# Performance work log

Hardware: AMD Instinct MI355X
Metric: run time of the kernel (lower is better)

## Reference

```python
import jax, jax.numpy as jnp
import numpy as np

HIDDEN = 2048
NUM_HEADS = 16
HEAD_DIM = HIDDEN // NUM_HEADS  # 128
ROPE_THETA = 10000.0
T = 4096


def _rope(x, positions):
    # x: [T, H, D]; neox-style rotary (rotate halves), matching vLLM get_rope default
    half = HEAD_DIM // 2
    inv_freq = 1.0 / (ROPE_THETA ** (jnp.arange(0, half, dtype=jnp.float32) / half))
    freqs = positions.astype(jnp.float32)[:, None] * inv_freq[None, :]  # [T, half]
    cos = jnp.cos(freqs)[:, None, :]  # [T, 1, half]
    sin = jnp.sin(freqs)[:, None, :]
    x1, x2 = x[..., :half], x[..., half:]
    return jnp.concatenate([x1 * cos - x2 * sin, x2 * cos + x1 * sin], axis=-1)


def setup_inputs() -> dict:
    key = jax.random.key(0)
    k1, k2, k3 = jax.random.split(key, 3)
    return {
        "hidden_states": jax.random.normal(k1, (T, HIDDEN), dtype=jnp.float32),
        "positions": jnp.arange(T, dtype=jnp.int32),
        "w_qkv": jax.random.normal(k2, (HIDDEN, 3 * HIDDEN), dtype=jnp.float32) * (HIDDEN ** -0.5),
        "w_o": jax.random.normal(k3, (HIDDEN, HIDDEN), dtype=jnp.float32) * (HIDDEN ** -0.5),
    }


def reference(hidden_states, positions, w_qkv, w_o):
    qkv = hidden_states @ w_qkv  # [T, 3H]
    q, k, v = jnp.split(qkv, 3, axis=-1)
    q = q.reshape(T, NUM_HEADS, HEAD_DIM)
    k = k.reshape(T, NUM_HEADS, HEAD_DIM)
    v = v.reshape(T, NUM_HEADS, HEAD_DIM)
    q = _rope(q, positions)
    k = _rope(k, positions)
    scale = HEAD_DIM ** -0.5
    # causal SDPA over flattened single sequence
    scores = jnp.einsum("qhd,khd->hqk", q, k) * scale  # [H, T, T]
    causal = jnp.tril(jnp.ones((T, T), dtype=bool))
    scores = jnp.where(causal[None, :, :], scores, jnp.finfo(scores.dtype).min)
    probs = jax.nn.softmax(scores, axis=-1)
    attn = jnp.einsum("hqk,khd->qhd", probs, v).reshape(T, HIDDEN)
    return attn @ w_o
```

## Files before the change

kernel.cpp:

```cpp
#include <hip/hip_runtime.h>
#include <hip/hip_bf16.h>
#include <cstdint>
#include <cstddef>

#define T_SEQ 4096
#define HID   2048
#define NH    16
#define HD    128
#define QKVN  6144
#define KVB   32
#define CHT   16
#define CPH   144

typedef unsigned short u16;
typedef unsigned int u32;
typedef __bf16 bf16x8 __attribute__((ext_vector_type(8)));
typedef float  f32x4  __attribute__((ext_vector_type(4)));

typedef const __attribute__((address_space(1))) void* gas_ptr;
typedef __attribute__((address_space(3))) void* las_ptr;

__device__ __forceinline__ void async16(const void* g, void* l) {
  __builtin_amdgcn_global_load_lds((gas_ptr)g, (las_ptr)l, 16, 0, 0);
}

__device__ __forceinline__ u16 f2bf(float f) {
  unsigned int u = __float_as_uint(f);
  u += 0x7fffu + ((u >> 16) & 1u);
  return (u16)(u >> 16);
}

__device__ __forceinline__ float bf2f(u16 x) {
  return __uint_as_float((unsigned)x << 16);
}

__global__ void cast_f32_bf16(const float* __restrict__ in, u16* __restrict__ out, int n) {
  int i = (blockIdx.x * blockDim.x + threadIdx.x) * 4;
  if (i >= n) return;
  float4 v = *(const float4*)&in[i];
  uint2 o;
  o.x = (unsigned)f2bf(v.x) | ((unsigned)f2bf(v.y) << 16);
  o.y = (unsigned)f2bf(v.z) | ((unsigned)f2bf(v.w) << 16);
  *(uint2*)&out[i] = o;
}

__global__ void transpose_cast(const float* __restrict__ in, u16* __restrict__ out,
                               int R, int C) {
  __shared__ float tile[64][65];
  int c0 = blockIdx.x * 64, r0 = blockIdx.y * 64;
  int tid = threadIdx.x;
#pragma unroll
  for (int i = 0; i < 16; ++i) {
    int e = i * 256 + tid;
    int rr = e >> 6, cc = e & 63;
    tile[rr][cc] = in[(size_t)(r0 + rr) * C + c0 + cc];
  }
  __syncthreads();
#pragma unroll
  for (int i = 0; i < 16; ++i) {
    int e = i * 256 + tid;
    int oc = e >> 6, orr = e & 63;
    out[(size_t)(c0 + oc) * R + r0 + orr] = f2bf(tile[orr][oc]);
  }
}

template <typename OUT>
__global__ __launch_bounds__(256)
void gemm_bf16_bt(const u16* __restrict__ A, const u16* __restrict__ BT,
                  OUT* __restrict__ C, int M, int N, int K) {
  __shared__ u16 As[2][128 * 32];
  __shared__ u16 Bs[2][128 * 32];
  int tid = threadIdx.x;
  int row0 = blockIdx.y * 128, col0 = blockIdx.x * 128;
  int wv = tid >> 6, lane = tid & 63, lr = lane & 15, lq = lane >> 4;
  int wm = (wv >> 1) * 64, wn = (wv & 1) * 64;
  f32x4 acc[4][4] = {};

  auto stage = [&](int buf, int ks) {
#pragma unroll
    for (int k = 0; k < 2; ++k) {
      int c = k * 256 + tid;
      int row = c >> 2, col = c & 3;
      int key = (row >> 1) & 3;
      async16(&A[(size_t)(row0 + row) * K + ks + (col ^ key) * 8], &As[buf][c * 8]);
      async16(&BT[(size_t)(col0 + row) * K + ks + (col ^ key) * 8], &Bs[buf][c * 8]);
    }
  };

  stage(0, 0);
  __syncthreads();
  int nk = K >> 5;
  for (int t = 0; t < nk; ++t) {
    int cur = t & 1;
    if (t + 1 < nk) stage(cur ^ 1, (t + 1) * 32);

    const char* AsB = (const char*)&As[cur][0];
    const char* BsB = (const char*)&Bs[cur][0];
    bf16x8 a[4], b[4];
#pragma unroll
    for (int mi = 0; mi < 4; ++mi) {
      int row = wm + mi * 16 + lr;
      a[mi] = *(const bf16x8*)(AsB + row * 64 + ((lq ^ ((row >> 1) & 3)) << 4));
    }
#pragma unroll
    for (int ni = 0; ni < 4; ++ni) {
      int row = wn + ni * 16 + lr;
      b[ni] = *(const bf16x8*)(BsB + row * 64 + ((lq ^ ((row >> 1) & 3)) << 4));
    }
#pragma unroll
    for (int mi = 0; mi < 4; ++mi)
#pragma unroll
      for (int ni = 0; ni < 4; ++ni)
        acc[mi][ni] = __builtin_amdgcn_mfma_f32_16x16x32_bf16(a[mi], b[ni], acc[mi][ni], 0, 0, 0);
    __syncthreads();
  }

#pragma unroll
  for (int mi = 0; mi < 4; ++mi)
#pragma unroll
    for (int ni = 0; ni < 4; ++ni)
#pragma unroll
      for (int r = 0; r < 4; ++r) {
        float v = acc[mi][ni][r];
        size_t idx = (size_t)(row0 + wm + mi * 16 + lq * 4 + r) * N + col0 + wn + ni * 16 + lr;
        if constexpr (sizeof(OUT) == 2) C[idx] = (OUT)f2bf(v);
        else                            C[idx] = (OUT)v;
      }
}

#define SCL2 0.12753224f

__global__ void rope_reorg(const u16* __restrict__ qkv, const int* __restrict__ pos,
                           u16* __restrict__ Qh, u16* __restrict__ Kh) {
  int idx = blockIdx.x * 256 + threadIdx.x;
  if (idx >= T_SEQ * NH * 64) return;
  int d = idx & 63;
  int h = (idx >> 6) & (NH - 1);
  int t = idx >> 10;
  float p = (float)pos[t];
  float inv = exp2f((float)d * -0.20762050594046932f);
  float f = p * inv;
  float s, c;
  __sincosf(f, &s, &c);

  size_t ib = (size_t)t * QKVN + h * HD + d;
  float q1 = bf2f(qkv[ib]), q2 = bf2f(qkv[ib + 64]);
  float k1 = bf2f(qkv[ib + HID]), k2 = bf2f(qkv[ib + HID + 64]);
  size_t ob = ((size_t)h * T_SEQ + t) * HD + d;
  Qh[ob]      = f2bf((q1 * c - q2 * s) * SCL2);
  Qh[ob + 64] = f2bf((q2 * c + q1 * s) * SCL2);
  Kh[ob]      = f2bf(k1 * c - k2 * s);
  Kh[ob + 64] = f2bf(k2 * c + k1 * s);
}

__global__ void vtrans(const u16* __restrict__ qkv, u16* __restrict__ Vt) {
  __shared__ u16 tile[64][136];
  int t0 = blockIdx.x * 64;
  int h = blockIdx.y;
  int tid = threadIdx.x;
#pragma unroll
  for (int i = 0; i < 32; ++i) {
    int e = i * 256 + tid;
    int tt = e >> 7, d = e & 127;
    tile[tt][d] = qkv[(size_t)(t0 + tt) * QKVN + 2 * HID + h * HD + d];
  }
  __syncthreads();
#pragma unroll
  for (int i = 0; i < 32; ++i) {
    int e = i * 256 + tid;
    int d = e >> 6, tt = e & 63;
    Vt[((size_t)h * HD + d) * T_SEQ + t0 + tt] = tile[tt][d];
  }
}

__global__ __launch_bounds__(256)
void attn_fwd(const u16* __restrict__ Qh, const u16* __restrict__ Kh,
              const u16* __restrict__ Vt, u16* __restrict__ Opart,
              float2* __restrict__ ml) {
  __shared__ u16 Ks[2][32 * 128];
  __shared__ u16 Vs[2][128 * 32];
  __shared__ u16 Ps[4][32 * 32];

  int tid = threadIdx.x;
  int wv = tid >> 6, lane = tid & 63, lr = lane & 15, lq = lane >> 4;
  char* PsB = (char*)&Ps[wv][0];

  int id = blockIdx.x;
  int h = id / CPH;
  int w = id - h * CPH;
  int bq = 0, acc = 0;
  for (;;) {
    int ch = (bq + 4) >> 2;
    if (w < acc + ch) break;
    acc += ch;
    ++bq;
  }
  int c = w - acc;
  int nt = 4 * bq + 4;
  int j0 = c * CHT, j1 = min(j0 + CHT, nt);
  int q0 = bq * 128, wrow0 = q0 + wv * 32;

  bf16x8 qf[2][4];
#pragma unroll
  for (int mi = 0; mi < 2; ++mi)
#pragma unroll
    for (int kd = 0; kd < 4; ++kd)
      qf[mi][kd] = *(const bf16x8*)
          &Qh[((size_t)h * T_SEQ + wrow0 + mi * 16 + lr) * HD + kd * 32 + lq * 8];

  f32x4 acc_o[2][8] = {};
  float m_run[2][4], l_run[2][4];
#pragma unroll
  for (int mi = 0; mi < 2; ++mi)
#pragma unroll
    for (int r = 0; r < 4; ++r) { m_run[mi][r] = -1e30f; l_run[mi][r] = 0.0f; }

  auto stage = [&](int buf, int jb) {
#pragma unroll
    for (int k = 0; k < 2; ++k) {
      int cc = k * 256 + tid;
      int row = cc >> 4;
      int sc = (cc ^ (row & 7)) & 15;
      async16(&Kh[((size_t)h * T_SEQ + jb + row) * HD + sc * 8], &Ks[buf][cc * 8]);
    }
#pragma unroll
    for (int k = 0; k < 2; ++k) {
      int cc = k * 256 + tid;
      int row = cc >> 2, col = cc & 3;
      int key = (row >> 1) & 3;
      async16(&Vt[((size_t)h * HD + row) * T_SEQ + jb + (col ^ key) * 8],
              &Vs[buf][cc * 8]);
    }
  };

  stage(0, j0 * KVB);
  __syncthreads();

  for (int j = j0; j < j1; ++j) {
    int cur = (j - j0) & 1;
    int jb = j * KVB;
    if (j + 1 < j1) stage(cur ^ 1, jb + KVB);

    if (jb <= wrow0 + 31) {
      const char* KsB = (const char*)&Ks[cur][0];
      const char* VsB = (const char*)&Vs[cur][0];

      f32x4 s_acc[2][2] = {};
#pragma unroll
      for (int kd = 0; kd < 4; ++kd) {
#pragma unroll
        for (int nj = 0; nj < 2; ++nj) {
          int row = nj * 16 + lr;
          int byt = (row << 8) + kd * 64 + lq * 16;
          bf16x8 kf = *(const bf16x8*)(KsB + (byt ^ ((row & 7) << 4)));
#pragma unroll
          for (int mi = 0; mi < 2; ++mi)
            s_acc[mi][nj] = __builtin_amdgcn_mfma_f32_16x16x32_bf16(
                qf[mi][kd], kf, s_acc[mi][nj], 0, 0, 0);
        }
      }

      bool diag = (jb + KVB - 1 > wrow0);
#pragma unroll
      for (int mi = 0; mi < 2; ++mi) {
        float pm[4];
#pragma unroll
        for (int r = 0; r < 4; ++r) {
          int qrow = wrow0 + mi * 16 + lq * 4 + r;
          float mx = -1e30f;
#pragma unroll
          for (int nj = 0; nj < 2; ++nj) {
            float sv = s_acc[mi][nj][r];
            if (diag && (jb + nj * 16 + lr > qrow)) sv = -1e30f;
            s_acc[mi][nj][r] = sv;
            mx = fmaxf(mx, sv);
          }
          pm[r] = mx;
        }
#pragma unroll
        for (int r = 0; r < 4; ++r) {
          pm[r] = fmaxf(pm[r], __shfl_xor(pm[r], 1));
          pm[r] = fmaxf(pm[r], __shfl_xor(pm[r], 2));
          pm[r] = fmaxf(pm[r], __shfl_xor(pm[r], 4));
          pm[r] = fmaxf(pm[r], __shfl_xor(pm[r], 8));
        }
#pragma unroll
        for (int r = 0; r < 4; ++r) {
          float mnew = fmaxf(m_run[mi][r], pm[r]);
          float sf = exp2f(m_run[mi][r] - mnew);
          m_run[mi][r] = mnew;
          int prow = mi * 16 + lq * 4 + r;
          float rs = 0.0f;
#pragma unroll
          for (int nj = 0; nj < 2; ++nj) {
            float p = exp2f(s_acc[mi][nj][r] - mnew);
            rs += p;
            *(u16*)(PsB + prow * 64 + (((nj * 16 + lr) * 2) ^ ((prow & 3) << 4))) = f2bf(p);
          }
          l_run[mi][r] = l_run[mi][r] * sf + rs;
#pragma unroll
          for (int nd = 0; nd < 8; ++nd) acc_o[mi][nd][r] *= sf;
        }
      }

#pragma unroll
      for (int mi = 0; mi < 2; ++mi) {
        int prow = mi * 16 + lr;
        bf16x8 pa = *(const bf16x8*)(PsB + prow * 64 + ((lq ^ (prow & 3)) << 4));
#pragma unroll
        for (int nd = 0; nd < 8; ++nd) {
          int vrow = nd * 16 + lr;
          bf16x8 vb = *(const bf16x8*)(VsB + vrow * 64 + ((lq ^ ((vrow >> 1) & 3)) << 4));
          acc_o[mi][nd] = __builtin_amdgcn_mfma_f32_16x16x32_bf16(
              pa, vb, acc_o[mi][nd], 0, 0, 0);
        }
      }
    }
    __syncthreads();
  }

  u16* Op = Opart + (size_t)id * 128 * 128;
#pragma unroll
  for (int mi = 0; mi < 2; ++mi)
#pragma unroll
    for (int r = 0; r < 4; ++r) {
      float l = l_run[mi][r];
      l += __shfl_xor(l, 1);
      l += __shfl_xor(l, 2);
      l += __shfl_xor(l, 4);
      l += __shfl_xor(l, 8);
      int rowl = wv * 32 + mi * 16 + lq * 4 + r;
#pragma unroll
      for (int nd = 0; nd < 8; ++nd)
        Op[rowl * 128 + nd * 16 + lr] = f2bf(acc_o[mi][nd][r]);
      if (lr == 0)
        ml[(size_t)id * 128 + rowl] = make_float2(m_run[mi][r], l);
    }
}

__global__ __launch_bounds__(256)
void attn_combine(const u16* __restrict__ Opart, const float2* __restrict__ ml,
                  u16* __restrict__ attn) {
  int idx = blockIdx.x * 256 + threadIdx.x;
  int e8 = idx * 8;
  int qrow = e8 >> 11;
  int col = e8 & (HID - 1);
  int h = col >> 7, coll = col & 127;
  int bq = qrow >> 7, ql = qrow & 127;
  int a = bq >> 2, r = bq & 3;
  int base = h * CPH + (a + 1) * (2 * a + r);
  int n = (bq + 4) >> 2;

  float m = -1e30f;
  for (int c = 0; c < n; ++c) m = fmaxf(m, ml[(size_t)(base + c) * 128 + ql].x);
  float lsum = 0.0f;
  float o[8] = {};
  for (int c = 0; c < n; ++c) {
    float2 mlc = ml[(size_t)(base + c) * 128 + ql];
    float wgt = exp2f(mlc.x - m);
    lsum += mlc.y * wgt;
    const u16* src = Opart + ((size_t)(base + c) * 128 + ql) * 128 + coll;
    ushort4 v0 = *(const ushort4*)src;
    ushort4 v1 = *(const ushort4*)(src + 4);
    o[0] += bf2f(v0.x) * wgt; o[1] += bf2f(v0.y) * wgt;
    o[2] += bf2f(v0.z) * wgt; o[3] += bf2f(v0.w) * wgt;
    o[4] += bf2f(v1.x) * wgt; o[5] += bf2f(v1.y) * wgt;
    o[6] += bf2f(v1.z) * wgt; o[7] += bf2f(v1.w) * wgt;
  }
  float rl = 1.0f / lsum;
  uint4 w;
  w.x = (u32)f2bf(o[0] * rl) | ((u32)f2bf(o[1] * rl) << 16);
  w.y = (u32)f2bf(o[2] * rl) | ((u32)f2bf(o[3] * rl) << 16);
  w.z = (u32)f2bf(o[4] * rl) | ((u32)f2bf(o[5] * rl) << 16);
  w.w = (u32)f2bf(o[6] * rl) | ((u32)f2bf(o[7] * rl) << 16);
  *(uint4*)&attn[e8] = w;
}

extern "C" void kernel_launch(void* const* d_in, const int* in_sizes, int n_in,
                              void* d_out, int out_size, void* d_ws, size_t ws_size,
                              hipStream_t stream) {
  const float* hidden    = (const float*)d_in[0];
  const int*   positions = (const int*)d_in[1];
  const float* w_qkv     = (const float*)d_in[2];
  const float* w_o       = (const float*)d_in[3];
  float* out = (float*)d_out;

  char* p = (char*)d_ws;
  u16* woT    = (u16*)p;  p += (size_t)HID * HID * 2;
  u16* Qh     = (u16*)p;  p += (size_t)T_SEQ * HID * 2;
  u16* Kh     = (u16*)p;  p += (size_t)T_SEQ * HID * 2;
  u16* Vt     = (u16*)p;  p += (size_t)T_SEQ * HID * 2;
  u16* attn_b = (u16*)p;  p += (size_t)T_SEQ * HID * 2;
  char* un = p;
  u16* hs_b   = (u16*)un;
  u16* wqkvT  = (u16*)(un + (size_t)T_SEQ * HID * 2);
  u16* qkvb   = (u16*)(un + (size_t)T_SEQ * HID * 2 + (size_t)QKVN * HID * 2);
  u16* Opart  = (u16*)un;
  float2* ml  = (float2*)(un + (size_t)NH * CPH * 128 * 128 * 2);

  cast_f32_bf16<<<(T_SEQ * HID / 4 + 255) / 256, 256, 0, stream>>>(hidden, hs_b, T_SEQ * HID);
  transpose_cast<<<dim3(QKVN / 64, HID / 64), 256, 0, stream>>>(w_qkv, wqkvT, HID, QKVN);
  transpose_cast<<<dim3(HID / 64, HID / 64), 256, 0, stream>>>(w_o, woT, HID, HID);
  gemm_bf16_bt<u16><<<dim3(QKVN / 128, T_SEQ / 128), 256, 0, stream>>>(hs_b, wqkvT, qkvb,
                                                                       T_SEQ, QKVN, HID);
  rope_reorg<<<(T_SEQ * NH * 64 + 255) / 256, 256, 0, stream>>>(qkvb, positions, Qh, Kh);
  vtrans<<<dim3(T_SEQ / 64, NH), 256, 0, stream>>>(qkvb, Vt);
  attn_fwd<<<NH * CPH, 256, 0, stream>>>(Qh, Kh, Vt, Opart, ml);
  attn_combine<<<T_SEQ * HID / 8 / 256, 256, 0, stream>>>(Opart, ml, attn_b);
  gemm_bf16_bt<float><<<dim3(HID / 128, T_SEQ / 128), 256, 0, stream>>>(attn_b, woT, out,
                                                                        T_SEQ, HID, HID);
}
```

Before: 456.9 us.

## Compute transposed S tile so each lane owns one query row for softmax

The QK^T MFMA now computes S^T (K as A operand, Q as B), so each lane holds one query row across four key columns. Online-softmax state collapses to one max and sum per lane, and the row reduction needs only two cross-lane shuffles instead of four per row. P is written to LDS as packed 8-byte stores rather than scalar 16-bit stores. The rescale factor must then be broadcast back to the PV accumulator layout with extra shuffles, which adds some cross-lane traffic.

```diff
diff --git a/kernel.cpp b/kernel.cpp
--- a/kernel.cpp
+++ b/kernel.cpp
@@ -202,18 +202,15 @@
 
   bf16x8 qf[2][4];
 #pragma unroll
-  for (int mi = 0; mi < 2; ++mi)
+  for (int qi = 0; qi < 2; ++qi)
 #pragma unroll
     for (int kd = 0; kd < 4; ++kd)
-      qf[mi][kd] = *(const bf16x8*)
-          &Qh[((size_t)h * T_SEQ + wrow0 + mi * 16 + lr) * HD + kd * 32 + lq * 8];
+      qf[qi][kd] = *(const bf16x8*)
+          &Qh[((size_t)h * T_SEQ + wrow0 + qi * 16 + lr) * HD + kd * 32 + lq * 8];
 
   f32x4 acc_o[2][8] = {};
-  float m_run[2][4], l_run[2][4];
-#pragma unroll
-  for (int mi = 0; mi < 2; ++mi)
-#pragma unroll
-    for (int r = 0; r < 4; ++r) { m_run[mi][r] = -1e30f; l_run[mi][r] = 0.0f; }
+  float m_run[2] = {-1e30f, -1e30f};
+  float l_run[2] = {0.0f, 0.0f};
 
   auto stage = [&](int buf, int jb) {
 #pragma unroll
@@ -245,68 +242,79 @@
       const char* KsB = (const char*)&Ks[cur][0];
       const char* VsB = (const char*)&Vs[cur][0];
 
-      f32x4 s_acc[2][2] = {};
+      f32x4 st[2][2] = {};
 #pragma unroll
       for (int kd = 0; kd < 4; ++kd) {
 #pragma unroll
-        for (int nj = 0; nj < 2; ++nj) {
-          int row = nj * 16 + lr;
+        for (int kj = 0; kj < 2; ++kj) {
+          int row = kj * 16 + lr;
           int byt = (row << 8) + kd * 64 + lq * 16;
           bf16x8 kf = *(const bf16x8*)(KsB + (byt ^ ((row & 7) << 4)));
 #pragma unroll
-          for (int mi = 0; mi < 2; ++mi)
-            s_acc[mi][nj] = __builtin_amdgcn_mfma_f32_16x16x32_bf16(
-                qf[mi][kd], kf, s_acc[mi][nj], 0, 0, 0);
+          for (int qi = 0; qi < 2; ++qi)
+            st[kj][qi] = __builtin_amdgcn_mfma_f32_16x16x32_bf16(
+                kf, qf[qi][kd], st[kj][qi], 0, 0, 0);
         }
       }
 
-      bool diag = (jb + KVB - 1 > wrow0);
+      if (jb + KVB - 1 > wrow0) {
+#pragma unroll
+        for (int qi = 0; qi < 2; ++qi) {
+          int qg = wrow0 + qi * 16 + lr;
+#pragma unroll
+          for (int kj = 0; kj < 2; ++kj)
+#pragma unroll
+            for (int r = 0; r < 4; ++r)
+              if (jb + kj * 16 + lq * 4 + r > qg) st[kj][qi][r] = -1e30f;
+        }
+      }
+
+      float sf[2];
+#pragma unroll
+      for (int qi = 0; qi < 2; ++qi) {
+        float mx = fmaxf(fmaxf(fmaxf(st[0][qi][0], st[0][qi][1]),
+                               fmaxf(st[0][qi][2], st[0][qi][3])),
+                         fmaxf(fmaxf(st[1][qi][0], st[1][qi][1]),
+                               fmaxf(st[1][qi][2], st[1][qi][3])));
+        mx = fmaxf(mx, __shfl_xor(mx, 16));
+        mx = fmaxf(mx, __shfl_xor(mx, 32));
+        float mnew = fmaxf(m_run[qi], mx);
+        sf[qi] = exp2f(m_run[qi] - mnew);
+        m_run[qi] = mnew;
+
+        int rowb = (qi * 16 + lr) * 64;
+        int key = ((lr >> 1) & 3) << 4;
+        float rs = 0.0f;
+#pragma unroll
+        for (int kj = 0; kj < 2; ++kj) {
+          float p0 = exp2f(st[kj][qi][0] - mnew);
+          float p1 = exp2f(st[kj][qi][1] - mnew);
+          float p2 = exp2f(st[kj][qi][2] - mnew);
+          float p3 = exp2f(st[kj][qi][3] - mnew);
+          rs += (p0 + p1) + (p2 + p3);
+          uint2 wq;
+          wq.x = (u32)f2bf(p0) | ((u32)f2bf(p1) << 16);
+          wq.y = (u32)f2bf(p2) | ((u32)f2bf(p3) << 16);
+          *(uint2*)(PsB + rowb + (((kj * 16 + lq * 4) * 2) ^ key)) = wq;
+        }
+        l_run[qi] = l_run[qi] * sf[qi] + rs;
+      }
+
 #pragma unroll
       for (int mi = 0; mi < 2; ++mi) {
-        float pm[4];
-#pragma unroll
-        for (int r = 0; r < 4; ++r) {
-          int qrow = wrow0 + mi * 16 + lq * 4 + r;
-          float mx = -1e30f;
-#pragma unroll
-          for (int nj = 0; nj < 2; ++nj) {
-            float sv = s_acc[mi][nj][r];
-            if (diag && (jb + nj * 16 + lr > qrow)) sv = -1e30f;
-            s_acc[mi][nj][r] = sv;
-            mx = fmaxf(mx, sv);
-          }
-          pm[r] = mx;
-        }
-#pragma unroll
-        for (int r = 0; r < 4; ++r) {
-          pm[r] = fmaxf(pm[r], __shfl_xor(pm[r], 1));
-          pm[r] = fmaxf(pm[r], __shfl_xor(pm[r], 2));
-          pm[r] = fmaxf(pm[r], __shfl_xor(pm[r], 4));
-          pm[r] = fmaxf(pm[r], __shfl_xor(pm[r], 8));
-        }
-#pragma unroll
-        for (int r = 0; r < 4; ++r) {
-          float mnew = fmaxf(m_run[mi][r], pm[r]);
-          float sf = exp2f(m_run[mi][r] - mnew);
-          m_run[mi][r] = mnew;
-          int prow = mi * 16 + lq * 4 + r;
-          float rs = 0.0f;
-#pragma unroll
-          for (int nj = 0; nj < 2; ++nj) {
-            float p = exp2f(s_acc[mi][nj][r] - mnew);
-            rs += p;
-            *(u16*)(PsB + prow * 64 + (((nj * 16 + lr) * 2) ^ ((prow & 3) << 4))) = f2bf(p);
-          }
-          l_run[mi][r] = l_run[mi][r] * sf + rs;
-#pragma unroll
-          for (int nd = 0; nd < 8; ++nd) acc_o[mi][nd][r] *= sf;
-        }
+        float sfb[4];
+#pragma unroll
+        for (int r = 0; r < 4; ++r) sfb[r] = __shfl(sf[mi], lq * 4 + r);
+#pragma unroll
+        for (int nd = 0; nd < 8; ++nd)
+#pragma unroll
+          for (int r = 0; r < 4; ++r) acc_o[mi][nd][r] *= sfb[r];
       }
 
 #pragma unroll
       for (int mi = 0; mi < 2; ++mi) {
         int prow = mi * 16 + lr;
-        bf16x8 pa = *(const bf16x8*)(PsB + prow * 64 + ((lq ^ (prow & 3)) << 4));
+        bf16x8 pa = *(const bf16x8*)(PsB + prow * 64 + ((lq ^ ((lr >> 1) & 3)) << 4));
 #pragma unroll
         for (int nd = 0; nd < 8; ++nd) {
           int vrow = nd * 16 + lr;
@@ -321,21 +329,22 @@
 
   u16* Op = Opart + (size_t)id * 128 * 128;
 #pragma unroll
-  for (int mi = 0; mi < 2; ++mi)
+  for (int mi = 0; mi < 2; ++mi) {
+    float l = l_run[mi];
+    l += __shfl_xor(l, 16);
+    l += __shfl_xor(l, 32);
+    if (lq == 0) {
+      int rowl = wv * 32 + mi * 16 + lr;
+      ml[(size_t)id * 128 + rowl] = make_float2(m_run[mi], l);
+    }
 #pragma unroll
     for (int r = 0; r < 4; ++r) {
-      float l = l_run[mi][r];
-      l += __shfl_xor(l, 1);
-      l += __shfl_xor(l, 2);
-      l += __shfl_xor(l, 4);
-      l += __shfl_xor(l, 8);
       int rowl = wv * 32 + mi * 16 + lq * 4 + r;
 #pragma unroll
       for (int nd = 0; nd < 8; ++nd)
         Op[rowl * 128 + nd * 16 + lr] = f2bf(acc_o[mi][nd][r]);
-      if (lr == 0)
-        ml[(size_t)id * 128 + rowl] = make_float2(m_run[mi][r], l);
-    }
+    }
+  }
 }
 
 __global__ __launch_bounds__(256)
```

New measurement: 416.3 us. 8.9% less time.
